# Performance work log

Measured on AMD Instinct MI355X. Metric: run time of the kernel, lower is better.

## Reference

```python
import jax, jax.numpy as jnp
import numpy as np

NUM_EMBEDDINGS = 8192
EMBEDDING_DIM = 64


def setup_inputs() -> dict:
    key = jax.random.key(0)
    k1, k2 = jax.random.split(key)
    hidden_states = jax.random.normal(k1, (32, EMBEDDING_DIM, 32, 32), dtype=jnp.float32)
    # nn.Embedding weight initialized uniform(-1/K, 1/K)
    bound = 1.0 / NUM_EMBEDDINGS
    emb_weight = jax.random.uniform(
        k2, (NUM_EMBEDDINGS, EMBEDDING_DIM), dtype=jnp.float32,
        minval=-bound, maxval=bound,
    )
    return {"hidden_states": hidden_states, "emb_weight": emb_weight}


def reference(hidden_states, emb_weight):
    # NCHW -> NHWC
    x = jnp.transpose(hidden_states, (0, 2, 3, 1))  # [B, H, W, C]
    B, H, W, C = x.shape
    x_flat = x.reshape(-1, C)  # [N, C]
    inputs_norm_sq = jnp.sum(x_flat * x_flat, axis=1, keepdims=True)  # [N, 1]
    codebook_norm_sq = jnp.sum(emb_weight * emb_weight, axis=1)  # [K]
    distances = inputs_norm_sq + codebook_norm_sq[None, :] - 2.0 * (x_flat @ emb_weight.T)  # [N, K]
    min_encoding_indices = jnp.argmin(distances, axis=1)  # [N]
    # one-hot matmul lookup == gather of codebook rows
    z_q = emb_weight[min_encoding_indices].reshape(B, H, W, C)
    z_q = jnp.transpose(z_q, (0, 3, 1, 2))  # back to NCHW
    indices = min_encoding_indices.reshape(B, H * W)
    return z_q, indices
```

## Files before the change

### kernel.cpp

```cpp
#include <hip/hip_runtime.h>
#include <math.h>


#define DIM      64
#define NCODE    8192
#define NROWS    32768
#define RPB      128
#define KQ       2048
#define CHUNK    128
#define NCHUNK   (KQ / CHUNK)
#define SEED_CH  2
#define HALF_DELTA 4.0e-5f
#define CAP_W    768

typedef __attribute__((ext_vector_type(8))) short frag8;
typedef __attribute__((ext_vector_type(4))) float f32x4;

__device__ __forceinline__ unsigned short f2bf_rne(float f) {
  unsigned u = __float_as_uint(f);
  return (unsigned short)((u + 0x7FFFu + ((u >> 16) & 1u)) >> 16);
}

__global__ __launch_bounds__(256) void xpose(const float* __restrict__ x,
                                             float* __restrict__ xT) {
  __shared__ float t[64][65];
  const int b = blockIdx.x >> 4, hw0 = (blockIdx.x & 15) << 6;
  const float* xb = x + (size_t)b * (DIM * 1024) + hw0;
  const int r = threadIdx.x & 63, c0 = threadIdx.x >> 6;
#pragma unroll
  for (int cc = 0; cc < DIM; cc += 4)
    t[r][cc + c0] = xb[(size_t)(cc + c0) * 1024 + r];
  __syncthreads();
  float* o = xT + (size_t)(b * 1024 + hw0) * DIM;
#pragma unroll
  for (int it = 0; it < 4; ++it) {
    const int idx = it * 256 + threadIdx.x;
    const int row = idx >> 4, j = (idx & 15) << 2;
    float4 v = {t[row][j], t[row][j + 1], t[row][j + 2], t[row][j + 3]};
    *(float4*)(o + row * DIM + j) = v;
  }
}

__global__ __launch_bounds__(256) void cvt_emb(const float* __restrict__ emb,
                                               unsigned short* __restrict__ ebf) {
  const int i = (blockIdx.x * 256 + threadIdx.x) * 8;
  const float4 a = *(const float4*)(emb + i);
  const float4 c = *(const float4*)(emb + i + 4);
  union { unsigned short u[8]; uint4 v; } o;
  o.u[0] = f2bf_rne(a.x); o.u[1] = f2bf_rne(a.y);
  o.u[2] = f2bf_rne(a.z); o.u[3] = f2bf_rne(a.w);
  o.u[4] = f2bf_rne(c.x); o.u[5] = f2bf_rne(c.y);
  o.u[6] = f2bf_rne(c.z); o.u[7] = f2bf_rne(c.w);
  *(uint4*)(ebf + i) = o.v;
}

__global__ __launch_bounds__(256) void vq_main(
    const float* __restrict__ x, const float* __restrict__ emb,
    const unsigned short* __restrict__ ebf, const float* __restrict__ xT,
    unsigned long long* __restrict__ wsbest)
{
  __shared__ uint4 ldsB[CHUNK * 8];
  __shared__ float s_normx[RPB];
  __shared__ unsigned long long s_best[RPB];
  __shared__ unsigned s_candw[4][CAP_W];

  const int tid  = threadIdx.x;
  const int lane = tid & 63;
  const int wave = tid >> 6;
  const int s    = lane & 15;
  const int q    = lane >> 4;
  const int rowbase = blockIdx.x * RPB;
  const int kbase   = blockIdx.y * KQ;
  const int b    = rowbase >> 10;
  const int hw0  = rowbase & 1023;
  const float* xb = x + (size_t)b * (DIM * 1024);

  if (tid < RPB) {
    s_best[tid] = ~0ull;
    float p[DIM];
#pragma unroll
    for (int c = 0; c < DIM; ++c) {
      const float v = xb[(size_t)c * 1024 + hw0 + tid];
      p[c] = __fmul_rn(v, v);
    }
    float r8[8];
#pragma unroll
    for (int j = 0; j < 8; ++j) {
      float ss = p[j];
#pragma unroll
      for (int m = 1; m < 8; ++m) ss = __fadd_rn(ss, p[m * 8 + j]);
      r8[j] = ss;
    }
    const float t0 = __fadd_rn(r8[0], r8[1]), t1 = __fadd_rn(r8[2], r8[3]);
    const float t2 = __fadd_rn(r8[4], r8[5]), t3 = __fadd_rn(r8[6], r8[7]);
    s_normx[tid] = __fadd_rn(__fadd_rn(t0, t1), __fadd_rn(t2, t3));
  }

  frag8 afr[2][2];
#pragma unroll
  for (int rt = 0; rt < 2; ++rt) {
    const float* xp = xb + hw0 + wave * 32 + rt * 16 + s;
#pragma unroll
    for (int h = 0; h < 2; ++h) {
      frag8 f;
#pragma unroll
      for (int j = 0; j < 8; ++j)
        f[j] = (short)f2bf_rne(xp[(size_t)(h * 32 + q * 8 + j) * 1024]);
      afr[rt][h] = f;
    }
  }

  const int lbA = s * 8 + ((q)     ^ (s & 7));
  const int lbB = s * 8 + ((4 + q) ^ (s & 7));
  const frag8* ldsF = (const frag8*)ldsB;

  f32x4 smax[2];
#pragma unroll
  for (int rt = 0; rt < 2; ++rt) smax[rt] = (f32x4){-1e30f, -1e30f, -1e30f, -1e30f};

#pragma unroll 1
  for (int ch = 0; ch < SEED_CH; ++ch) {
    __syncthreads();
    {
      const int code = tid >> 1, half = tid & 1;
      const uint4* src = (const uint4*)(ebf + (size_t)(kbase + ch * CHUNK + code) * DIM) + half * 4;
      const int sw = code & 7;
#pragma unroll
      for (int j = 0; j < 4; ++j) ldsB[code * 8 + ((half * 4 + j) ^ sw)] = src[j];
    }
    __syncthreads();
#pragma unroll
    for (int t = 0; t < 8; ++t) {
      const frag8 b0 = ldsF[lbA + t * 128];
      const frag8 b1 = ldsF[lbB + t * 128];
#pragma unroll
      for (int rt = 0; rt < 2; ++rt) {
        f32x4 d = {0.f, 0.f, 0.f, 0.f};
        d = __builtin_amdgcn_mfma_f32_16x16x32_bf16(afr[rt][0], b0, d, 0, 0, 0);
        d = __builtin_amdgcn_mfma_f32_16x16x32_bf16(afr[rt][1], b1, d, 0, 0, 0);
        smax[rt][0] = fmaxf(smax[rt][0], d[0]);
        smax[rt][1] = fmaxf(smax[rt][1], d[1]);
        smax[rt][2] = fmaxf(smax[rt][2], d[2]);
        smax[rt][3] = fmaxf(smax[rt][3], d[3]);
      }
    }
  }

  float thr[2][4];
#pragma unroll
  for (int rt = 0; rt < 2; ++rt)
#pragma unroll
    for (int r = 0; r < 4; ++r) {
      float v = smax[rt][r];
      v = fmaxf(v, __shfl_xor(v, 1, 64));
      v = fmaxf(v, __shfl_xor(v, 2, 64));
      v = fmaxf(v, __shfl_xor(v, 4, 64));
      v = fmaxf(v, __shfl_xor(v, 8, 64));
      thr[rt][r] = v - HALF_DELTA;
    }

  int wcnt = 0;
  for (int ch = 0; ch < NCHUNK; ++ch) {
    __syncthreads();
    {
      const int code = tid >> 1, half = tid & 1;
      const uint4* src = (const uint4*)(ebf + (size_t)(kbase + ch * CHUNK + code) * DIM) + half * 4;
      const int sw = code & 7;
#pragma unroll
      for (int j = 0; j < 4; ++j) ldsB[code * 8 + ((half * 4 + j) ^ sw)] = src[j];
    }
    __syncthreads();
#pragma unroll
    for (int t = 0; t < 8; ++t) {
      const frag8 b0 = ldsF[lbA + t * 128];
      const frag8 b1 = ldsF[lbB + t * 128];
      const int kl = ch * CHUNK + t * 16 + s;
#pragma unroll
      for (int rt = 0; rt < 2; ++rt) {
        f32x4 d = {0.f, 0.f, 0.f, 0.f};
        d = __builtin_amdgcn_mfma_f32_16x16x32_bf16(afr[rt][0], b0, d, 0, 0, 0);
        d = __builtin_amdgcn_mfma_f32_16x16x32_bf16(afr[rt][1], b1, d, 0, 0, 0);
#pragma unroll
        for (int r = 0; r < 4; ++r) {
          const bool pr = d[r] >= thr[rt][r];
          const unsigned long long m = __ballot(pr);
          if (m) {
            const int off = __builtin_amdgcn_mbcnt_hi(
                (unsigned)(m >> 32),
                __builtin_amdgcn_mbcnt_lo((unsigned)m, 0u));
            if (pr) {
              const int pos = wcnt + off;
              if (pos < CAP_W)
                s_candw[wave][pos] =
                    ((unsigned)(rt * 16 + q * 4 + r) << 11) | (unsigned)kl;
            }
            wcnt += __builtin_popcountll(m);
          }
        }
      }
    }
  }

  const int wc = min(wcnt, CAP_W);
  for (int i = lane; i < wc; i += 64) {
    const unsigned e = s_candw[wave][i];
    const int row_l = wave * 32 + (int)(e >> 11);
    const int kg = kbase + (int)(e & 0x7FFu);
    const float* ep = emb + (size_t)kg * DIM;
    const float* xp = xT + (size_t)(rowbase + row_l) * DIM;
    float S = 0.f;
#pragma unroll
    for (int c = 0; c < DIM; ++c) S = __fmaf_rn(xp[c], ep[c], S);
    const float dd = __fsub_rn(s_normx[row_l], __fadd_rn(S, S));
    const unsigned long long pack =
        ((unsigned long long)__float_as_uint(dd) << 13) | (unsigned long long)kg;
    atomicMin(&s_best[row_l], pack);
  }
  __syncthreads();

  if (tid < RPB)
    wsbest[(size_t)(rowbase + tid) * 4 + blockIdx.y] = s_best[tid];
}

__global__ __launch_bounds__(256) void vq_out(
    const float* __restrict__ emb, const unsigned long long* __restrict__ wsbest,
    float* __restrict__ zq, float* __restrict__ idx_out)
{
  const int row = blockIdx.x * 256 + threadIdx.x;
  unsigned long long p = wsbest[(size_t)row * 4];
#pragma unroll
  for (int j = 1; j < 4; ++j) {
    const unsigned long long pj = wsbest[(size_t)row * 4 + j];
    if (pj < p) p = pj;
  }
  const int k = (int)(p & 0x1FFFull);
  idx_out[row] = (float)k;
  const int b = row >> 10, hw = row & 1023;
  const float* ep = emb + (size_t)k * DIM;
  float* zp = zq + (size_t)b * (DIM * 1024) + hw;
#pragma unroll
  for (int c = 0; c < DIM; ++c) zp[(size_t)c * 1024] = ep[c];
}

extern "C" void kernel_launch(void* const* d_in, const int* in_sizes, int n_in,
                              void* d_out, int out_size, void* d_ws, size_t ws_size,
                              hipStream_t stream) {
  const float* x   = (const float*)d_in[0];
  const float* emb = (const float*)d_in[1];

  float* zq      = (float*)d_out;
  float* idx_out = zq + (size_t)NROWS * DIM;

  unsigned short*     ebf    = (unsigned short*)d_ws;
  unsigned long long* wsbest = (unsigned long long*)((char*)d_ws + (1 << 20));

  float* xT = zq;

  xpose<<<dim3(512), 256, 0, stream>>>(x, xT);
  cvt_emb<<<dim3(256), 256, 0, stream>>>(emb, ebf);
  vq_main<<<dim3(NROWS / RPB, 4), 256, 0, stream>>>(x, emb, ebf, xT, wsbest);
  vq_out<<<dim3(NROWS / 256), 256, 0, stream>>>(emb, wsbest, zq, idx_out);
}
```

Baseline: 206.0 us.

## Tighten candidate threshold per chunk, fuse prep kernels, vectorize rescoring loads

The running per-row maximum of the approximate dot product is now updated during the main scan, and the pruning threshold is refreshed after every chunk. This means fewer candidates should pass into the fp32 rescoring phase. The transpose and bf16 codebook conversion are merged into a single prep kernel to save one launch. The fp32 rescore loop now reads with float4 loads. The trade-off is extra fmax and shuffle-reduction work on every chunk.

```diff
diff --git a/kernel.cpp b/kernel.cpp
--- a/kernel.cpp
+++ b/kernel.cpp
@@ -21,8 +21,21 @@
   return (unsigned short)((u + 0x7FFFu + ((u >> 16) & 1u)) >> 16);
 }
 
-__global__ __launch_bounds__(256) void xpose(const float* __restrict__ x,
-                                             float* __restrict__ xT) {
+__global__ __launch_bounds__(256) void prep(const float* __restrict__ x,
+                                            float* __restrict__ xT,
+                                            const float* __restrict__ emb,
+                                            unsigned short* __restrict__ ebf) {
+  if (blockIdx.x < 256) {
+    const int i = (blockIdx.x * 256 + threadIdx.x) * 8;
+    const float4 a = *(const float4*)(emb + i);
+    const float4 c = *(const float4*)(emb + i + 4);
+    union { unsigned short u[8]; uint4 v; } o;
+    o.u[0] = f2bf_rne(a.x); o.u[1] = f2bf_rne(a.y);
+    o.u[2] = f2bf_rne(a.z); o.u[3] = f2bf_rne(a.w);
+    o.u[4] = f2bf_rne(c.x); o.u[5] = f2bf_rne(c.y);
+    o.u[6] = f2bf_rne(c.z); o.u[7] = f2bf_rne(c.w);
+    *(uint4*)(ebf + i) = o.v;
+  }
   __shared__ float t[64][65];
   const int b = blockIdx.x >> 4, hw0 = (blockIdx.x & 15) << 6;
   const float* xb = x + (size_t)b * (DIM * 1024) + hw0;
@@ -39,19 +52,6 @@
     float4 v = {t[row][j], t[row][j + 1], t[row][j + 2], t[row][j + 3]};
     *(float4*)(o + row * DIM + j) = v;
   }
-}
-
-__global__ __launch_bounds__(256) void cvt_emb(const float* __restrict__ emb,
-                                               unsigned short* __restrict__ ebf) {
-  const int i = (blockIdx.x * 256 + threadIdx.x) * 8;
-  const float4 a = *(const float4*)(emb + i);
-  const float4 c = *(const float4*)(emb + i + 4);
-  union { unsigned short u[8]; uint4 v; } o;
-  o.u[0] = f2bf_rne(a.x); o.u[1] = f2bf_rne(a.y);
-  o.u[2] = f2bf_rne(a.z); o.u[3] = f2bf_rne(a.w);
-  o.u[4] = f2bf_rne(c.x); o.u[5] = f2bf_rne(c.y);
-  o.u[6] = f2bf_rne(c.z); o.u[7] = f2bf_rne(c.w);
-  *(uint4*)(ebf + i) = o.v;
 }
 
 __global__ __launch_bounds__(256) void vq_main(
@@ -197,8 +197,23 @@
             wcnt += __builtin_popcountll(m);
           }
         }
+        smax[rt][0] = fmaxf(smax[rt][0], d[0]);
+        smax[rt][1] = fmaxf(smax[rt][1], d[1]);
+        smax[rt][2] = fmaxf(smax[rt][2], d[2]);
+        smax[rt][3] = fmaxf(smax[rt][3], d[3]);
       }
     }
+#pragma unroll
+    for (int rt = 0; rt < 2; ++rt)
+#pragma unroll
+      for (int r = 0; r < 4; ++r) {
+        float v = smax[rt][r];
+        v = fmaxf(v, __shfl_xor(v, 1, 64));
+        v = fmaxf(v, __shfl_xor(v, 2, 64));
+        v = fmaxf(v, __shfl_xor(v, 4, 64));
+        v = fmaxf(v, __shfl_xor(v, 8, 64));
+        thr[rt][r] = v - HALF_DELTA;
+      }
   }
 
   const int wc = min(wcnt, CAP_W);
@@ -206,11 +221,18 @@
     const unsigned e = s_candw[wave][i];
     const int row_l = wave * 32 + (int)(e >> 11);
     const int kg = kbase + (int)(e & 0x7FFu);
-    const float* ep = emb + (size_t)kg * DIM;
-    const float* xp = xT + (size_t)(rowbase + row_l) * DIM;
+    const float4* ep4 = (const float4*)(emb + (size_t)kg * DIM);
+    const float4* xp4 = (const float4*)(xT + (size_t)(rowbase + row_l) * DIM);
     float S = 0.f;
 #pragma unroll
-    for (int c = 0; c < DIM; ++c) S = __fmaf_rn(xp[c], ep[c], S);
+    for (int c4 = 0; c4 < DIM / 4; ++c4) {
+      const float4 e4 = ep4[c4];
+      const float4 x4 = xp4[c4];
+      S = __fmaf_rn(x4.x, e4.x, S);
+      S = __fmaf_rn(x4.y, e4.y, S);
+      S = __fmaf_rn(x4.z, e4.z, S);
+      S = __fmaf_rn(x4.w, e4.w, S);
+    }
     const float dd = __fsub_rn(s_normx[row_l], __fadd_rn(S, S));
     const unsigned long long pack =
         ((unsigned long long)__float_as_uint(dd) << 13) | (unsigned long long)kg;
@@ -256,8 +278,7 @@
 
   float* xT = zq;
 
-  xpose<<<dim3(512), 256, 0, stream>>>(x, xT);
-  cvt_emb<<<dim3(256), 256, 0, stream>>>(emb, ebf);
+  prep<<<dim3(512), 256, 0, stream>>>(x, xT, emb, ebf);
   vq_main<<<dim3(NROWS / RPB, 4), 256, 0, stream>>>(x, emb, ebf, xT, wsbest);
   vq_out<<<dim3(NROWS / 256), 256, 0, stream>>>(emb, wsbest, zq, idx_out);
 }
```

Measured after the change: 225.9 us. 1.1x slower.
